# Kernel optimization log

Measured on AMD Instinct MI355X. Metric: run time of the kernel, lower is better.

Reference implementation:

```python
import jax, jax.numpy as jnp
import numpy as np

B, T, N = 512, 1024, 48


def setup_inputs() -> dict:
    key = jax.random.key(0)
    k1, k2, k3, k4 = jax.random.split(key, 4)
    potentials = jax.random.normal(k1, (B, T, N), dtype=jnp.float32)
    y_true = jax.random.randint(k2, (B, T), 0, N, dtype=jnp.int32)
    lengths = jax.random.randint(k3, (B,), 1, T + 1, dtype=jnp.int32)
    transitions = jax.random.normal(k4, (N, N), dtype=jnp.float32)
    return {"potentials": potentials, "y_true": y_true,
            "lengths": lengths, "transitions": transitions}


def _crf_log_likelihood(potentials, tags, lengths, trans):
    # potentials: [B,T,N], tags: [B,T] int, lengths: [B] int, trans: [N,N]
    Bv, Tv, Nv = potentials.shape
    t_idx = jnp.arange(Tv)

    # ---- numerator: score of the given tag sequence ----
    unary = jnp.take_along_axis(potentials, tags[..., None], axis=2)[..., 0]  # [B,T]
    unary_mask = (t_idx[None, :] < lengths[:, None]).astype(potentials.dtype)
    unary_score = jnp.sum(unary * unary_mask, axis=1)  # [B]

    trans_scores = trans[tags[:, :-1], tags[:, 1:]]  # [B,T-1]
    pair_mask = (t_idx[None, 1:] < lengths[:, None]).astype(potentials.dtype)
    binary_score = jnp.sum(trans_scores * pair_mask, axis=1)  # [B]
    seq_score = unary_score + binary_score

    # ---- log partition: forward algorithm with length masking ----
    alpha0 = potentials[:, 0, :]  # [B,N]
    pots_rest = jnp.transpose(potentials[:, 1:, :], (1, 0, 2))  # [T-1,B,N]
    valid = (t_idx[1:, None] < lengths[None, :])  # [T-1,B]

    def step(alpha, inp):
        pot_t, v = inp  # [B,N], [B]
        # logsumexp over previous state: alpha[b,i] + trans[i,j]
        new_alpha = jax.nn.logsumexp(alpha[:, :, None] + trans[None, :, :], axis=1) + pot_t
        alpha = jnp.where(v[:, None], new_alpha, alpha)
        return alpha, None

    alpha_final, _ = jax.lax.scan(step, alpha0, (pots_rest, valid))
    log_norm = jax.nn.logsumexp(alpha_final, axis=-1)  # [B]

    return seq_score - log_norm


def reference(potentials, y_true, lengths, transitions):
    ll = _crf_log_likelihood(potentials, y_true.astype(jnp.int32),
                             lengths.astype(jnp.int32), transitions)
    return -ll  # per-sample NLL, shape [B]
```

## Files before the change

kernel.cpp:

```cpp
#include <hip/hip_runtime.h>
#include <cstdint>
#include <cstddef>

constexpr int Bb = 512;
constexpr int Tt = 1024;
constexpr int Nn = 48;
constexpr int SG = 16;
constexpr int NG = Bb / SG;
constexpr int Cc = 32;
constexpr int Lc = Tt / Cc;
constexpr int Wb = 32;
constexpr int AP = 72;

typedef short bf16x8 __attribute__((ext_vector_type(8)));
typedef float f32x4  __attribute__((ext_vector_type(4)));

__device__ __forceinline__ unsigned short bf16_rne(float x) {
    const unsigned int u = __float_as_uint(x);
    return (unsigned short)((u + 0x7FFFu + ((u >> 16) & 1u)) >> 16);
}
__device__ __forceinline__ float safe_log(float x) {
    return __logf(fmaxf(x, 1e-30f));
}

__launch_bounds__(64, 1)
__global__ void crf_fused(const float* __restrict__ pot,
                          const int*   __restrict__ ytrue,
                          const int*   __restrict__ lengths,
                          const float* __restrict__ trans,
                          float*       __restrict__ out)
{
    __shared__ float trans_lds[Nn * Nn];
    __shared__ __align__(16) unsigned short ab[SG][AP];

    const int lane = threadIdx.x;
    const int ln   = lane & 15;
    const int q    = lane >> 4;
    const int gidx = blockIdx.x >> 5;
    const int c    = blockIdx.x & 31;
    const int s0   = gidx * SG;

    for (int i = lane; i < Nn * Nn; i += 64) trans_lds[i] = trans[i];
    for (int i = lane; i < SG * AP; i += 64) ((unsigned short*)ab)[i] = 0;
    __syncthreads();

    {
        const int    b    = blockIdx.x >> 1;
        const int    h    = blockIdx.x & 1;
        const int    lenb = lengths[b];
        const int*   yrow = ytrue + (size_t)b * Tt;
        const float* prow = pot + (size_t)b * Tt * Nn;
        float gold = 0.0f;
#pragma unroll
        for (int k = 0; k < Tt / 128; ++k) {
            const int   t    = h * (Tt / 2) + lane + 64 * k;
            const int   yt   = yrow[t];
            const int   ytm1 = yrow[(t > 0) ? (t - 1) : 0];
            const float u    = prow[(size_t)t * Nn + yt];
            const float tr   = trans_lds[ytm1 * Nn + yt];
            gold += (t < lenb) ? u : 0.0f;
            gold += (t >= 1 && t < lenb) ? tr : 0.0f;
        }
#pragma unroll
        for (int off = 32; off > 0; off >>= 1) gold += __shfl_xor(gold, off);
        if (lane == 0) atomicAdd(&out[b], -gold);
    }

    int len4[4];
#pragma unroll
    for (int r = 0; r < 4; ++r) len4[r] = lengths[s0 + q * 4 + r];
    int lmax = lengths[s0 + ln];
#pragma unroll
    for (int off = 8; off > 0; off >>= 1) {
        const int o = __shfl_xor(lmax, off);
        lmax = (o > lmax) ? o : lmax;
    }

    const int start = (c == 0) ? 1 : c * Lc;
    if (c > 0 && start >= lmax) return;
    const int end = ((c + 1) * Lc < lmax) ? (c + 1) * Lc : lmax;

    bf16x8 Bf[3][2];
#pragma unroll
    for (int nt = 0; nt < 3; ++nt)
#pragma unroll
        for (int kc = 0; kc < 2; ++kc)
#pragma unroll
            for (int d = 0; d < 8; ++d) {
                const int i = kc * 32 + q * 8 + d;
                const int j = nt * 16 + ln;
                const float v = (i < Nn) ? __expf(trans_lds[i * Nn + j]) : 0.0f;
                Bf[nt][kc][d] = (short)bf16_rne(v);
            }

    const float* pbase[4];
#pragma unroll
    for (int r = 0; r < 4; ++r)
        pbase[r] = pot + (size_t)(s0 + q * 4 + r) * (Tt * Nn) + ln;

    int t0 = (c == 0) ? 1 : (start - Wb);
    if (t0 < 1) t0 = 1;

    float pinit[3][4];
#pragma unroll
    for (int nt = 0; nt < 3; ++nt)
#pragma unroll
        for (int r = 0; r < 4; ++r)
            pinit[nt][r] = pbase[r][(size_t)(t0 - 1) * Nn + nt * 16];

    float sh4[4];
#pragma unroll
    for (int r = 0; r < 4; ++r) sh4[r] = __shfl(pinit[0][r], lane & 48);

    float prev[3][4];
    float gacc[4];
#pragma unroll
    for (int r = 0; r < 4; ++r) gacc[r] = (c == 0) ? sh4[r] : 0.0f;
#pragma unroll
    for (int nt = 0; nt < 3; ++nt)
#pragma unroll
        for (int r = 0; r < 4; ++r) {
            const float v = __expf(pinit[nt][r] - sh4[r]);
            prev[nt][r] = v;
            ab[q * 4 + r][nt * 16 + ln] = bf16_rne(v);
        }
    __builtin_amdgcn_sched_barrier(0);
    bf16x8 A0 = *(const bf16x8*)&ab[ln][q * 8];
    bf16x8 A1 = *(const bf16x8*)&ab[ln][32 + q * 8];
    __builtin_amdgcn_sched_barrier(0);

    float pbuf[4][3][4];
#pragma unroll
    for (int s = 0; s < 4; ++s) {
        const int ts = (t0 + s < Tt) ? (t0 + s) : (Tt - 1);
#pragma unroll
        for (int nt = 0; nt < 3; ++nt)
#pragma unroll
            for (int r = 0; r < 4; ++r)
                pbuf[s][nt][r] = pbase[r][(size_t)ts * Nn + nt * 16];
    }
    float epv[3][4];
#pragma unroll
    for (int nt = 0; nt < 3; ++nt)
#pragma unroll
        for (int r = 0; r < 4; ++r)
            epv[nt][r] = __expf(pbuf[0][nt][r]);

    const int ksteps = ((end - t0) + 3) & ~3;

#define CRF_STEP(KK, SS)                                                        \
    {                                                                           \
        const int t   = t0 + (KK);                                              \
        const int tld = (t + 4 < Tt) ? (t + 4) : (Tt - 1);                      \
        _Pragma("unroll")                                                       \
        for (int nt = 0; nt < 3; ++nt) {                                        \
            _Pragma("unroll")                                                   \
            for (int r = 0; r < 4; ++r)                                         \
                pbuf[SS][nt][r] = pbase[r][(size_t)tld * Nn + nt * 16];         \
        }                                                                       \
        f32x4 D[3];                                                             \
        _Pragma("unroll")                                                       \
        for (int nt = 0; nt < 3; ++nt) {                                        \
            f32x4 z = {0.0f, 0.0f, 0.0f, 0.0f};                                 \
            D[nt] = __builtin_amdgcn_mfma_f32_16x16x32_bf16(A0, Bf[nt][0], z, 0, 0, 0); \
            D[nt] = __builtin_amdgcn_mfma_f32_16x16x32_bf16(A1, Bf[nt][1], D[nt], 0, 0, 0); \
        }                                                                       \
        float vv[3][4];                                                         \
        _Pragma("unroll")                                                       \
        for (int nt = 0; nt < 3; ++nt) {                                        \
            _Pragma("unroll")                                                   \
            for (int r = 0; r < 4; ++r)                                         \
                vv[nt][r] = D[nt][r] * epv[nt][r];                              \
        }                                                                       \
        float c4[4];                                                            \
        _Pragma("unroll")                                                       \
        for (int r = 0; r < 4; ++r) c4[r] = __shfl(vv[0][r], lane & 48);        \
        float rr[4];                                                            \
        _Pragma("unroll")                                                       \
        for (int r = 0; r < 4; ++r) rr[r] = __builtin_amdgcn_rcpf(fmaxf(c4[r], 1e-30f)); \
        _Pragma("unroll")                                                       \
        for (int r = 0; r < 4; ++r) {                                           \
            const float lg = safe_log(c4[r]);                                   \
            gacc[r] += ((t >= start) && (t < len4[r]) && (t < end)) ? lg : 0.0f; \
        }                                                                       \
        _Pragma("unroll")                                                       \
        for (int nt = 0; nt < 3; ++nt) {                                        \
            _Pragma("unroll")                                                   \
            for (int r = 0; r < 4; ++r) {                                       \
                const float ns = (t < len4[r]) ? (vv[nt][r] * rr[r]) : prev[nt][r]; \
                prev[nt][r] = ns;                                               \
                ab[q * 4 + r][nt * 16 + ln] = bf16_rne(ns);                     \
            }                                                                   \
        }                                                                       \
        __builtin_amdgcn_sched_barrier(0);                                      \
        A0 = *(const bf16x8*)&ab[ln][q * 8];                                    \
        A1 = *(const bf16x8*)&ab[ln][32 + q * 8];                               \
        __builtin_amdgcn_sched_barrier(0);                                      \
        _Pragma("unroll")                                                       \
        for (int nt = 0; nt < 3; ++nt) {                                        \
            _Pragma("unroll")                                                   \
            for (int r = 0; r < 4; ++r)                                         \
                epv[nt][r] = __expf(pbuf[((SS) + 1) & 3][nt][r]);               \
        }                                                                       \
    }

    for (int k = 0; k < ksteps; k += 4) {
        CRF_STEP(k + 0, 0);
        CRF_STEP(k + 1, 1);
        CRF_STEP(k + 2, 2);
        CRF_STEP(k + 3, 3);
    }
#undef CRF_STEP

    float G[4];
#pragma unroll
    for (int r = 0; r < 4; ++r) {
        float rs = prev[0][r] + prev[1][r] + prev[2][r];
#pragma unroll
        for (int off = 8; off > 0; off >>= 1) rs += __shfl_xor(rs, off);
        const bool active_chunk = (c == 0) || (c * Lc < len4[r]);
        const bool last = active_chunk && (len4[r] <= (c + 1) * Lc);
        const float lgr = safe_log(rs);
        G[r] = gacc[r] + (last ? lgr : 0.0f);
    }
    if (ln == 0) {
#pragma unroll
        for (int r = 0; r < 4; ++r) atomicAdd(&out[s0 + q * 4 + r], G[r]);
    }
}

extern "C" void kernel_launch(void* const* d_in, const int* in_sizes, int n_in,
                              void* d_out, int out_size, void* d_ws, size_t ws_size,
                              hipStream_t stream)
{
    const float* pot   = (const float*)d_in[0];
    const int*   ytrue = (const int*)  d_in[1];
    const int*   lens  = (const int*)  d_in[2];
    const float* trans = (const float*)d_in[3];
    float*       out   = (float*)d_out;

    hipMemsetAsync(out, 0, (size_t)out_size * sizeof(float), stream);
    crf_fused<<<dim3(NG * Cc), dim3(64), 0, stream>>>(pot, ytrue, lens, trans, out);
}
```

Baseline: 195.2 us.

## Transpose CRF forward MFMA so alpha stays in registers, dropping LDS round-trip

Swaps the MFMA operand roles so the transition matrix is the A operand and the per-sequence alpha vector is the B operand, with state indices permuted so each lane's MFMA output maps directly into its next B fragment. The per-step LDS store/load of alpha through a shared buffer is replaced by in-register bf16 packing plus a few cross-lane shuffles. Potentials are loaded as float4 vectors per lane. Normalisation is deferred by folding the reciprocal into the next step's exp(potential) factor, with the log accumulation re-indexed to match. This shortens the serial per-timestep dependency chain at the cost of a subtle index permutation that must stay exactly consistent.

```diff
diff --git a/kernel.cpp b/kernel.cpp
--- a/kernel.cpp
+++ b/kernel.cpp
@@ -10,14 +10,17 @@
 constexpr int Cc = 32;
 constexpr int Lc = Tt / Cc;
 constexpr int Wb = 32;
-constexpr int AP = 72;
 
 typedef short bf16x8 __attribute__((ext_vector_type(8)));
 typedef float f32x4  __attribute__((ext_vector_type(4)));
-
-__device__ __forceinline__ unsigned short bf16_rne(float x) {
+typedef unsigned int u32x4 __attribute__((ext_vector_type(4)));
+
+__device__ __forceinline__ unsigned int bf16_rne(float x) {
     const unsigned int u = __float_as_uint(x);
-    return (unsigned short)((u + 0x7FFFu + ((u >> 16) & 1u)) >> 16);
+    return ((u + 0x7FFFu + ((u >> 16) & 1u)) >> 16);
+}
+__device__ __forceinline__ unsigned int pack2(float lo, float hi) {
+    return bf16_rne(lo) | (bf16_rne(hi) << 16);
 }
 __device__ __forceinline__ float safe_log(float x) {
     return __logf(fmaxf(x, 1e-30f));
@@ -31,7 +34,6 @@
                           float*       __restrict__ out)
 {
     __shared__ float trans_lds[Nn * Nn];
-    __shared__ __align__(16) unsigned short ab[SG][AP];
 
     const int lane = threadIdx.x;
     const int ln   = lane & 15;
@@ -41,7 +43,6 @@
     const int s0   = gidx * SG;
 
     for (int i = lane; i < Nn * Nn; i += 64) trans_lds[i] = trans[i];
-    for (int i = lane; i < SG * AP; i += 64) ((unsigned short*)ab)[i] = 0;
     __syncthreads();
 
     {
@@ -66,10 +67,8 @@
         if (lane == 0) atomicAdd(&out[b], -gold);
     }
 
-    int len4[4];
-#pragma unroll
-    for (int r = 0; r < 4; ++r) len4[r] = lengths[s0 + q * 4 + r];
-    int lmax = lengths[s0 + ln];
+    const int len_ln = lengths[s0 + ln];
+    int lmax = len_ln;
 #pragma unroll
     for (int off = 8; off > 0; off >>= 1) {
         const int o = __shfl_xor(lmax, off);
@@ -80,153 +79,149 @@
     if (c > 0 && start >= lmax) return;
     const int end = ((c + 1) * Lc < lmax) ? (c + 1) * Lc : lmax;
 
-    bf16x8 Bf[3][2];
+    bf16x8 Wf[3][2];
 #pragma unroll
     for (int nt = 0; nt < 3; ++nt)
 #pragma unroll
         for (int kc = 0; kc < 2; ++kc)
 #pragma unroll
             for (int d = 0; d < 8; ++d) {
-                const int i = kc * 32 + q * 8 + d;
-                const int j = nt * 16 + ln;
-                const float v = (i < Nn) ? __expf(trans_lds[i * Nn + j]) : 0.0f;
-                Bf[nt][kc][d] = (short)bf16_rne(v);
+                int i;
+                if (kc == 0) {
+                    i = 16 * (d >> 2) + 4 * q + (d & 3);
+                } else {
+                    i = (q < 2) ? (32 + 8 * q + d) : -1;
+                }
+                const float v = (i >= 0) ? __expf(trans_lds[i * Nn + nt * 16 + ln]) : 0.0f;
+                Wf[nt][kc][d] = (short)bf16_rne(v);
             }
 
-    const float* pbase[4];
-#pragma unroll
-    for (int r = 0; r < 4; ++r)
-        pbase[r] = pot + (size_t)(s0 + q * 4 + r) * (Tt * Nn) + ln;
+    const int slA = ((2 * q) & 3) * 16 + ln;
+    const int slB = slA + 16;
+    const int slC = ln;
+
+    const float* prow = pot + (size_t)(s0 + ln) * (Tt * Nn);
+    const float* pp0 = prow + 0 * 16 + q * 4;
+    const float* pp1 = prow + 1 * 16 + q * 4;
+    const float* pp2 = prow + 2 * 16 + q * 4;
 
     int t0 = (c == 0) ? 1 : (start - Wb);
     if (t0 < 1) t0 = 1;
 
-    float pinit[3][4];
-#pragma unroll
-    for (int nt = 0; nt < 3; ++nt)
-#pragma unroll
-        for (int r = 0; r < 4; ++r)
-            pinit[nt][r] = pbase[r][(size_t)(t0 - 1) * Nn + nt * 16];
-
-    float sh4[4];
-#pragma unroll
-    for (int r = 0; r < 4; ++r) sh4[r] = __shfl(pinit[0][r], lane & 48);
-
-    float prev[3][4];
-    float gacc[4];
-#pragma unroll
-    for (int r = 0; r < 4; ++r) gacc[r] = (c == 0) ? sh4[r] : 0.0f;
-#pragma unroll
-    for (int nt = 0; nt < 3; ++nt)
-#pragma unroll
-        for (int r = 0; r < 4; ++r) {
-            const float v = __expf(pinit[nt][r] - sh4[r]);
-            prev[nt][r] = v;
-            ab[q * 4 + r][nt * 16 + ln] = bf16_rne(v);
-        }
-    __builtin_amdgcn_sched_barrier(0);
-    bf16x8 A0 = *(const bf16x8*)&ab[ln][q * 8];
-    bf16x8 A1 = *(const bf16x8*)&ab[ln][32 + q * 8];
-    __builtin_amdgcn_sched_barrier(0);
-
-    float pbuf[4][3][4];
-#pragma unroll
-    for (int s = 0; s < 4; ++s) {
-        const int ts = (t0 + s < Tt) ? (t0 + s) : (Tt - 1);
-#pragma unroll
-        for (int nt = 0; nt < 3; ++nt)
-#pragma unroll
-            for (int r = 0; r < 4; ++r)
-                pbuf[s][nt][r] = pbase[r][(size_t)ts * Nn + nt * 16];
-    }
-    float epv[3][4];
-#pragma unroll
-    for (int nt = 0; nt < 3; ++nt)
-#pragma unroll
-        for (int r = 0; r < 4; ++r)
-            epv[nt][r] = __expf(pbuf[0][nt][r]);
+    f32x4 pin0 = *(const f32x4*)(pp0 + (size_t)(t0 - 1) * Nn);
+    f32x4 pin1 = *(const f32x4*)(pp1 + (size_t)(t0 - 1) * Nn);
+    f32x4 pin2 = *(const f32x4*)(pp2 + (size_t)(t0 - 1) * Nn);
+    const float cb0 = __shfl(pin0[0], slC);
+
+    float gacc = (c == 0) ? cb0 : 0.0f;
+    f32x4 prev0, prev1, prev2;
+#pragma unroll
+    for (int r = 0; r < 4; ++r) {
+        prev0[r] = __expf(pin0[r] - cb0);
+        prev1[r] = __expf(pin1[r] - cb0);
+        prev2[r] = __expf(pin2[r] - cb0);
+    }
+
+    unsigned int pk00 = pack2(prev0[0], prev0[1]);
+    unsigned int pk01 = pack2(prev0[2], prev0[3]);
+    unsigned int pk10 = pack2(prev1[0], prev1[1]);
+    unsigned int pk11 = pack2(prev1[2], prev1[3]);
+    unsigned int pk20 = pack2(prev2[0], prev2[1]);
+    unsigned int pk21 = pack2(prev2[2], prev2[3]);
+    bf16x8 Bf0 = __builtin_bit_cast(bf16x8, (u32x4){pk00, pk01, pk10, pk11});
+    bf16x8 Bf1 = __builtin_bit_cast(bf16x8, (u32x4){
+        (unsigned int)__shfl((int)pk20, slA), (unsigned int)__shfl((int)pk21, slA),
+        (unsigned int)__shfl((int)pk20, slB), (unsigned int)__shfl((int)pk21, slB)});
+
+    f32x4 P00, P01, P02, P10, P11, P12, P20, P21, P22, P30, P31, P32;
+    {
+        const size_t ta = (size_t)((t0 + 0 < Tt) ? t0 + 0 : Tt - 1) * Nn;
+        const size_t tb = (size_t)((t0 + 1 < Tt) ? t0 + 1 : Tt - 1) * Nn;
+        const size_t tc = (size_t)((t0 + 2 < Tt) ? t0 + 2 : Tt - 1) * Nn;
+        const size_t td = (size_t)((t0 + 3 < Tt) ? t0 + 3 : Tt - 1) * Nn;
+        P00 = *(const f32x4*)(pp0 + ta); P01 = *(const f32x4*)(pp1 + ta); P02 = *(const f32x4*)(pp2 + ta);
+        P10 = *(const f32x4*)(pp0 + tb); P11 = *(const f32x4*)(pp1 + tb); P12 = *(const f32x4*)(pp2 + tb);
+        P20 = *(const f32x4*)(pp0 + tc); P21 = *(const f32x4*)(pp1 + tc); P22 = *(const f32x4*)(pp2 + tc);
+        P30 = *(const f32x4*)(pp0 + td); P31 = *(const f32x4*)(pp1 + td); P32 = *(const f32x4*)(pp2 + td);
+    }
+    f32x4 epv0, epv1, epv2;
+#pragma unroll
+    for (int r = 0; r < 4; ++r) {
+        epv0[r] = __expf(P00[r]);
+        epv1[r] = __expf(P01[r]);
+        epv2[r] = __expf(P02[r]);
+    }
 
     const int ksteps = ((end - t0) + 3) & ~3;
 
-#define CRF_STEP(KK, SS)                                                        \
+#define CRF_STEP(KK, LA0, LA1, LA2, NB0, NB1, NB2)                              \
     {                                                                           \
         const int t   = t0 + (KK);                                              \
-        const int tld = (t + 4 < Tt) ? (t + 4) : (Tt - 1);                      \
-        _Pragma("unroll")                                                       \
-        for (int nt = 0; nt < 3; ++nt) {                                        \
-            _Pragma("unroll")                                                   \
-            for (int r = 0; r < 4; ++r)                                         \
-                pbuf[SS][nt][r] = pbase[r][(size_t)tld * Nn + nt * 16];         \
-        }                                                                       \
-        f32x4 D[3];                                                             \
-        _Pragma("unroll")                                                       \
-        for (int nt = 0; nt < 3; ++nt) {                                        \
-            f32x4 z = {0.0f, 0.0f, 0.0f, 0.0f};                                 \
-            D[nt] = __builtin_amdgcn_mfma_f32_16x16x32_bf16(A0, Bf[nt][0], z, 0, 0, 0); \
-            D[nt] = __builtin_amdgcn_mfma_f32_16x16x32_bf16(A1, Bf[nt][1], D[nt], 0, 0, 0); \
-        }                                                                       \
-        float vv[3][4];                                                         \
-        _Pragma("unroll")                                                       \
-        for (int nt = 0; nt < 3; ++nt) {                                        \
-            _Pragma("unroll")                                                   \
-            for (int r = 0; r < 4; ++r)                                         \
-                vv[nt][r] = D[nt][r] * epv[nt][r];                              \
-        }                                                                       \
-        float c4[4];                                                            \
-        _Pragma("unroll")                                                       \
-        for (int r = 0; r < 4; ++r) c4[r] = __shfl(vv[0][r], lane & 48);        \
-        float rr[4];                                                            \
-        _Pragma("unroll")                                                       \
-        for (int r = 0; r < 4; ++r) rr[r] = __builtin_amdgcn_rcpf(fmaxf(c4[r], 1e-30f)); \
+        const size_t tld = (size_t)((t + 4 < Tt) ? (t + 4) : (Tt - 1)) * Nn;    \
+        LA0 = *(const f32x4*)(pp0 + tld);                                       \
+        LA1 = *(const f32x4*)(pp1 + tld);                                       \
+        LA2 = *(const f32x4*)(pp2 + tld);                                       \
+        f32x4 z = {0.0f, 0.0f, 0.0f, 0.0f};                                     \
+        f32x4 D0 = __builtin_amdgcn_mfma_f32_16x16x32_bf16(Wf[0][0], Bf0, z, 0, 0, 0); \
+        f32x4 D1 = __builtin_amdgcn_mfma_f32_16x16x32_bf16(Wf[1][0], Bf0, z, 0, 0, 0); \
+        f32x4 D2 = __builtin_amdgcn_mfma_f32_16x16x32_bf16(Wf[2][0], Bf0, z, 0, 0, 0); \
+        D0 = __builtin_amdgcn_mfma_f32_16x16x32_bf16(Wf[0][1], Bf1, D0, 0, 0, 0); \
+        D1 = __builtin_amdgcn_mfma_f32_16x16x32_bf16(Wf[1][1], Bf1, D1, 0, 0, 0); \
+        D2 = __builtin_amdgcn_mfma_f32_16x16x32_bf16(Wf[2][1], Bf1, D2, 0, 0, 0); \
+        f32x4 a0, a1, a2;                                                       \
         _Pragma("unroll")                                                       \
         for (int r = 0; r < 4; ++r) {                                           \
-            const float lg = safe_log(c4[r]);                                   \
-            gacc[r] += ((t >= start) && (t < len4[r]) && (t < end)) ? lg : 0.0f; \
+            a0[r] = D0[r] * epv0[r];                                            \
+            a1[r] = D1[r] * epv1[r];                                            \
+            a2[r] = D2[r] * epv2[r];                                            \
         }                                                                       \
+        const float cb = __shfl(a0[0], slC);                                    \
+        const float rr = __builtin_amdgcn_rcpf(fmaxf(cb, 1e-30f));              \
+        const float lg = safe_log(cb);                                          \
+        gacc += ((t >= start) && (t < end) && (t + 1 < len_ln)) ? lg : 0.0f;    \
+        const bool act = (t < len_ln);                                          \
         _Pragma("unroll")                                                       \
-        for (int nt = 0; nt < 3; ++nt) {                                        \
-            _Pragma("unroll")                                                   \
-            for (int r = 0; r < 4; ++r) {                                       \
-                const float ns = (t < len4[r]) ? (vv[nt][r] * rr[r]) : prev[nt][r]; \
-                prev[nt][r] = ns;                                               \
-                ab[q * 4 + r][nt * 16 + ln] = bf16_rne(ns);                     \
-            }                                                                   \
+        for (int r = 0; r < 4; ++r) {                                           \
+            prev0[r] = act ? a0[r] : prev0[r];                                  \
+            prev1[r] = act ? a1[r] : prev1[r];                                  \
+            prev2[r] = act ? a2[r] : prev2[r];                                  \
         }                                                                       \
-        __builtin_amdgcn_sched_barrier(0);                                      \
-        A0 = *(const bf16x8*)&ab[ln][q * 8];                                    \
-        A1 = *(const bf16x8*)&ab[ln][32 + q * 8];                               \
-        __builtin_amdgcn_sched_barrier(0);                                      \
+        pk00 = pack2(prev0[0], prev0[1]);                                       \
+        pk01 = pack2(prev0[2], prev0[3]);                                       \
+        pk10 = pack2(prev1[0], prev1[1]);                                       \
+        pk11 = pack2(prev1[2], prev1[3]);                                       \
+        pk20 = pack2(prev2[0], prev2[1]);                                       \
+        pk21 = pack2(prev2[2], prev2[3]);                                       \
+        Bf0 = __builtin_bit_cast(bf16x8, (u32x4){pk00, pk01, pk10, pk11});      \
+        Bf1 = __builtin_bit_cast(bf16x8, (u32x4){                               \
+            (unsigned int)__shfl((int)pk20, slA), (unsigned int)__shfl((int)pk21, slA), \
+            (unsigned int)__shfl((int)pk20, slB), (unsigned int)__shfl((int)pk21, slB)}); \
         _Pragma("unroll")                                                       \
-        for (int nt = 0; nt < 3; ++nt) {                                        \
-            _Pragma("unroll")                                                   \
-            for (int r = 0; r < 4; ++r)                                         \
-                epv[nt][r] = __expf(pbuf[((SS) + 1) & 3][nt][r]);               \
+        for (int r = 0; r < 4; ++r) {                                           \
+            epv0[r] = __expf(NB0[r]) * rr;                                      \
+            epv1[r] = __expf(NB1[r]) * rr;                                      \
+            epv2[r] = __expf(NB2[r]) * rr;                                      \
         }                                                                       \
     }
 
     for (int k = 0; k < ksteps; k += 4) {
-        CRF_STEP(k + 0, 0);
-        CRF_STEP(k + 1, 1);
-        CRF_STEP(k + 2, 2);
-        CRF_STEP(k + 3, 3);
+        CRF_STEP(k + 0, P00, P01, P02, P10, P11, P12);
+        CRF_STEP(k + 1, P10, P11, P12, P20, P21, P22);
+        CRF_STEP(k + 2, P20, P21, P22, P30, P31, P32);
+        CRF_STEP(k + 3, P30, P31, P32, P00, P01, P02);
     }
 #undef CRF_STEP
 
-    float G[4];
-#pragma unroll
-    for (int r = 0; r < 4; ++r) {
-        float rs = prev[0][r] + prev[1][r] + prev[2][r];
-#pragma unroll
-        for (int off = 8; off > 0; off >>= 1) rs += __shfl_xor(rs, off);
-        const bool active_chunk = (c == 0) || (c * Lc < len4[r]);
-        const bool last = active_chunk && (len4[r] <= (c + 1) * Lc);
-        const float lgr = safe_log(rs);
-        G[r] = gacc[r] + (last ? lgr : 0.0f);
-    }
-    if (ln == 0) {
-#pragma unroll
-        for (int r = 0; r < 4; ++r) atomicAdd(&out[s0 + q * 4 + r], G[r]);
-    }
+    float rs = prev0[0] + prev0[1] + prev0[2] + prev0[3]
+             + prev1[0] + prev1[1] + prev1[2] + prev1[3]
+             + prev2[0] + prev2[1] + prev2[2] + prev2[3];
+    rs += __shfl_xor(rs, 16);
+    rs += __shfl_xor(rs, 32);
+
+    const bool active_chunk = (c == 0) || (c * Lc < len_ln);
+    const bool last = active_chunk && (len_ln <= (c + 1) * Lc);
+    const float G = gacc + (last ? safe_log(rs) : 0.0f);
+    if (lane < 16) atomicAdd(&out[s0 + ln], G);
 }
 
 extern "C" void kernel_launch(void* const* d_in, const int* in_sizes, int n_in,
```

Measured after the change: 182.0 us. 1.07x faster.
